# Optimization experiments

Measured on AMD Instinct MI355X. Metric: run time of the kernel, lower is better.

The kernel has to match this reference:

```python
import jax, jax.numpy as jnp
import numpy as np

B, T, V, E, H = 64, 1024, 50000, 256, 512


def setup_inputs() -> dict:
    key = jax.random.key(0)
    ks = jax.random.split(key, 4)
    x = jax.random.randint(ks[0], (B, T), 0, V, dtype=jnp.int32)  # 0 => masked (mask_zero=True)
    initialized_hidden = jnp.zeros((B, H), jnp.float32)
    initialized_cell = jnp.zeros((B, H), jnp.float32)
    emb = jax.random.normal(ks[1], (V, E), jnp.float32) * 0.05
    kernel = jax.random.normal(ks[2], (E, 4 * H), jnp.float32) / np.sqrt(E).astype(np.float32)
    rec_kernel = jax.random.normal(ks[3], (H, 4 * H), jnp.float32) / np.sqrt(H).astype(np.float32)
    # Keras LSTM default: zero bias with unit_forget_bias=True (forget gate bias = 1)
    bias = jnp.concatenate([jnp.zeros(H), jnp.ones(H), jnp.zeros(2 * H)]).astype(jnp.float32)
    return {"x": x, "initialized_hidden": initialized_hidden, "initialized_cell": initialized_cell,
            "emb": emb, "kernel": kernel, "rec_kernel": rec_kernel, "bias": bias}


def _masked_lstm(e, mask, h0, c0, rec_kernel, kernel, bias):
    # Precompute all input projections in one big GEMM: [T, B, 4H]
    xz = jnp.einsum('bte,eg->tbg', e, kernel) + bias
    m_t = mask.T  # [T, B]
    h_units = h0.shape[-1]

    def step(carry, inp):
        h, c = carry
        zx, mt = inp
        z = zx + h @ rec_kernel  # [B, 4H], gate order i,f,c,o (Keras)
        i = jax.nn.sigmoid(z[:, :h_units])
        f = jax.nn.sigmoid(z[:, h_units:2 * h_units])
        g = jnp.tanh(z[:, 2 * h_units:3 * h_units])
        o = jax.nn.sigmoid(z[:, 3 * h_units:])
        c_new = f * c + i * g
        h_new = o * jnp.tanh(c_new)
        m = mt[:, None]
        # masked steps: carry state & output through unchanged (Keras masking semantics)
        h = jnp.where(m, h_new, h)
        c = jnp.where(m, c_new, c)
        return (h, c), h

    (hT, cT), ys = jax.lax.scan(step, (h0, c0), (xz, m_t))
    return ys.transpose(1, 0, 2), hT, cT  # [B,T,H], [B,H], [B,H]


def reference(x, initialized_hidden, initialized_cell, emb, kernel, rec_kernel, bias):
    mask = x != 0  # mask_zero=True
    e = emb[x]     # [B, T, E] embedding lookup
    return _masked_lstm(e, mask, initialized_hidden, initialized_cell, rec_kernel, kernel, bias)
```

## Files before the change

### kernel.cpp

```cpp
#include <hip/hip_runtime.h>
#include <stdint.h>

typedef unsigned short u16;
typedef unsigned int u32;
typedef __attribute__((ext_vector_type(8))) short bf16x8;
typedef __attribute__((ext_vector_type(4))) float f32x4;
typedef __attribute__((ext_vector_type(4))) unsigned int u32x4;
typedef __attribute__((ext_vector_type(2))) unsigned int u32x2;

#define TT 1024
#define BB 64
#define EE 256
#define HH 512
#define GG 2048

#define AS1 __attribute__((address_space(1)))
#define AS3 __attribute__((address_space(3)))

__device__ __forceinline__ float bf2f(u16 h) {
  union { u32 i; float f; } v; v.i = ((u32)h) << 16; return v.f;
}
__device__ __forceinline__ u16 f2bf(float f) {
  union { float f; u32 i; } v; v.f = f;
  u32 b = v.i;
  return (u16)((b + 0x7fffu + ((b >> 16) & 1u)) >> 16);
}
__device__ __forceinline__ float sigm(float x) {
  return 1.f / (1.f + __expf(-x));
}
__device__ __forceinline__ float tanhfast(float x) {
  float e = __expf(2.f * x);
  return 1.f - 2.f / (e + 1.f);
}
__device__ __forceinline__ int cellpos8(int bl, int u) {
  return ((u >> 5) * 32 + ((bl & 7) | (((u >> 3) & 3) << 3))) * 8 + (u & 7);
}
__device__ __forceinline__ int rowbad(u32x4 v, u32 e) {
  return ((((v[0] ^ e) | (v[1] ^ e)) | ((v[2] ^ e) | (v[3] ^ e))) & 0xffffu)
         != 0;
}

#define LOADF(dst, ptr)                                              \
  asm volatile("global_load_dwordx4 %0, %1, off sc0"                 \
               : "=v"(dst) : "v"(ptr))
#define LOADS(dst, ptr)                                              \
  asm volatile("global_load_dwordx4 %0, %1, off sc0 sc1"             \
               : "=v"(dst) : "v"(ptr))
#define WAITV0                                                       \
  asm volatile("s_waitcnt vmcnt(0)" ::: "memory");                   \
  __builtin_amdgcn_sched_barrier(0)

__global__ __launch_bounds__(256) void conv_emb(const float* __restrict__ emb,
                                                u16* __restrict__ embbf) {
  int i = blockIdx.x * 256 + threadIdx.x;
  float4 v = ((const float4*)emb)[i];
  u32x2 p;
  p[0] = (u32)f2bf(v.x) | ((u32)f2bf(v.y) << 16);
  p[1] = (u32)f2bf(v.z) | ((u32)f2bf(v.w) << 16);
  ((u32x2*)embbf)[i] = p;
}

__global__ __launch_bounds__(256) void pack_wk(const float* __restrict__ Wk,
                                               u16* __restrict__ wkp) {
  int idx = blockIdx.x * 256 + threadIdx.x;
  int ct = idx >> 9, ks = (idx >> 6) & 7, l = idx & 63;
  int col = ct * 16 + (l & 15);
  int kb = ks * 32 + ((l >> 4) << 3);
  u32x4 p;
#pragma unroll
  for (int h = 0; h < 4; ++h) {
    u16 a = f2bf(Wk[(size_t)(kb + 2 * h) * GG + col]);
    u16 b = f2bf(Wk[(size_t)(kb + 2 * h + 1) * GG + col]);
    p[h] = (u32)a | ((u32)b << 16);
  }
  *(u32x4*)&wkp[(size_t)idx * 8] = p;
}

__global__ __launch_bounds__(512) void xz_gemm2(
    const int* __restrict__ x, const u16* __restrict__ embbf,
    const u16* __restrict__ wkp, const float* __restrict__ bias,
    u16* __restrict__ xz) {
  extern __shared__ char smg[];
  __shared__ int xidx[16][64];
  __shared__ float biasl[256];
  const int tid = threadIdx.x;
  const int wv = tid >> 6, l = tid & 63;
  const int cb = blockIdx.x & 7;
  const int tg = blockIdx.x >> 3;
  const int mt = wv & 3, nh = wv >> 2;

#pragma unroll
  for (int i = 0; i < 16; ++i)
    __builtin_amdgcn_global_load_lds(
        (AS1 const u32*)(wkp + ((size_t)cb * 65536) +
                         (size_t)(((i * 8 + wv) * 64) + l) * 8),
        (AS3 u32*)(smg + ((i * 8 + wv) << 10)), 16, 0, 0);
  if (tid < 256) {
    int b = tid >> 2, k4 = (tid & 3) << 2;
    int4 v = *(const int4*)&x[(size_t)b * TT + tg * 16 + k4];
    xidx[k4 + 0][b] = v.x; xidx[k4 + 1][b] = v.y;
    xidx[k4 + 2][b] = v.z; xidx[k4 + 3][b] = v.w;
    biasl[tid] = bias[cb * 256 + tid];
  }
  __syncthreads();

  const int row = mt * 16 + (l & 15);
  const int b0 = mt * 16 + ((l >> 4) << 2);
  for (int tl = 0; tl < 16; ++tl) {
    const int xid = xidx[tl][row];
    bf16x8 af[8];
#pragma unroll
    for (int ks = 0; ks < 8; ++ks)
      af[ks] = *(const bf16x8*)&embbf[(size_t)xid * EE + ks * 32 +
                                      ((l >> 4) << 3)];
    const int t = tg * 16 + tl;
#pragma unroll
    for (int nt = 0; nt < 8; ++nt) {
      const int ctl = nh * 8 + nt;
      f32x4 acc = {0.f, 0.f, 0.f, 0.f};
#pragma unroll
      for (int ks = 0; ks < 8; ++ks)
        acc = __builtin_amdgcn_mfma_f32_16x16x32_bf16(
            af[ks], *(const bf16x8*)(smg + (((ctl * 8 + ks) * 64 + l) << 4)),
            acc, 0, 0, 0);
      const int col = cb * 256 + ctl * 16 + (l & 15);
      const float bj = biasl[ctl * 16 + (l & 15)];
      u16 o0 = f2bf(acc[0] + bj), o1 = f2bf(acc[1] + bj);
      u16 o2 = f2bf(acc[2] + bj), o3 = f2bf(acc[3] + bj);
      u32* dst = (u32*)(xz + ((size_t)t * GG + col) * BB + b0);
      dst[0] = (u32)o0 | ((u32)o1 << 16);
      dst[1] = (u32)o2 | ((u32)o3 << 16);
    }
  }
}

__global__ __launch_bounds__(256) void xz_gemm_mfma(
    const int* __restrict__ x, const float* __restrict__ emb,
    const float* __restrict__ Wk, const float* __restrict__ bias,
    u16* __restrict__ xz) {
  extern __shared__ char sm1[];
  bf16x8* Bl = (bf16x8*)sm1;
  __shared__ int xidx[64];
  const int tid = threadIdx.x;
  const int t = blockIdx.x;
  const int w = tid >> 6, l = tid & 63;
  if (tid < 64) xidx[tid] = x[(size_t)tid * TT + t];
  __syncthreads();
  const int row = w * 16 + (l & 15);
  const int xid = xidx[row];
  bf16x8 af[8];
#pragma unroll
  for (int ks = 0; ks < 8; ++ks) {
    int k0 = ks * 32 + ((l >> 4) << 3);
    const float4* p = (const float4*)(emb + (size_t)xid * EE + k0);
    float4 a0 = p[0], a1 = p[1];
    bf16x8 v;
    v[0] = (short)f2bf(a0.x); v[1] = (short)f2bf(a0.y);
    v[2] = (short)f2bf(a0.z); v[3] = (short)f2bf(a0.w);
    v[4] = (short)f2bf(a1.x); v[5] = (short)f2bf(a1.y);
    v[6] = (short)f2bf(a1.z); v[7] = (short)f2bf(a1.w);
    af[ks] = v;
  }
  for (int nb = 0; nb < 8; ++nb) {
    __syncthreads();
    for (int idx = tid; idx < 8192; idx += 256) {
      int nt = idx >> 9, ks = (idx >> 6) & 7, l2 = idx & 63;
      int col = nb * 256 + nt * 16 + (l2 & 15);
      int kb = ks * 32 + ((l2 >> 4) << 3);
      bf16x8 v;
#pragma unroll
      for (int j = 0; j < 8; ++j)
        v[j] = (short)f2bf(Wk[(size_t)(kb + j) * GG + col]);
      Bl[idx] = v;
    }
    __syncthreads();
#pragma unroll 2
    for (int nt = 0; nt < 16; ++nt) {
      f32x4 acc = {0.f, 0.f, 0.f, 0.f};
#pragma unroll
      for (int ks = 0; ks < 8; ++ks)
        acc = __builtin_amdgcn_mfma_f32_16x16x32_bf16(
            af[ks], Bl[(nt * 8 + ks) * 64 + l], acc, 0, 0, 0);
      int col = nb * 256 + nt * 16 + (l & 15);
      float bj = bias[col];
      int b0 = w * 16 + ((l >> 4) << 2);
      u16 o0 = f2bf(acc[0] + bj), o1 = f2bf(acc[1] + bj);
      u16 o2 = f2bf(acc[2] + bj), o3 = f2bf(acc[3] + bj);
      u32* dst = (u32*)(xz + ((size_t)t * GG + col) * BB + b0);
      dst[0] = (u32)o0 | ((u32)o1 << 16);
      dst[1] = (u32)o2 | ((u32)o3 << 16);
    }
  }
}

__global__ __launch_bounds__(512, 2) void lstm_scan12(
    const int* __restrict__ x, const float* __restrict__ h0,
    const float* __restrict__ c0, const float* __restrict__ rec,
    const u16* __restrict__ xz, float* __restrict__ out,
    u32* __restrict__ fastb, u32* __restrict__ slowb) {
  extern __shared__ char sm2[];
  u16* A0 = (u16*)sm2;
  u16* A1 = (u16*)(sm2 + 8192);
  u32* xmask = (u32*)(sm2 + 16384);
  char* ring = sm2 + 17408;
  const int tid = threadIdx.x;
  const int wv = tid >> 6, l = tid & 63;
  const int g = blockIdx.x & 7;
  const int r = blockIdx.x >> 3;
  const int Bg = g * 8;
  const int U0 = r * 64;
  const int q = l & 3;
  const int uoff = (l >> 2) & 3;
  const int u0g = U0 + 8 * wv + uoff;
  const int u1g = u0g + 4;
  const int col0 = q * 512 + u0g;
  const int col1 = q * 512 + u1g;
  const int bl = ((l >> 4) << 2) + q;
  const int blc = bl & 7;
  const bool act = (l < 32);
  const int b = Bg + blc;
  u32* FP0 = fastb + (g * 2 + 0) * 4096;
  u32* FP1 = fastb + (g * 2 + 1) * 4096;
  u32* SP0 = slowb + (g * 2 + 0) * 4096;
  u32* SP1 = slowb + (g * 2 + 1) * 4096;

  const size_t gofs = ((size_t)(wv * 512 + U0 + l)) * BB + Bg;
  if (wv < 4) {
#pragma unroll
    for (int s = 0; s < 7; ++s)
      __builtin_amdgcn_global_load_lds(
          (AS1 const u32*)(xz + (size_t)s * GG * BB + gofs),
          (AS3 u32*)(ring + s * 4096 + wv * 1024), 16, 0, 0);
  }

  bf16x8 bfr0[16], bfr1[16];
#pragma unroll
  for (int ks = 0; ks < 16; ++ks) {
    int kbase = ks * 32 + ((l >> 4) << 3);
#pragma unroll
    for (int j = 0; j < 8; ++j) {
      bfr0[ks][j] = (short)f2bf(rec[(size_t)(kbase + j) * GG + col0]);
      bfr1[ks][j] = (short)f2bf(rec[(size_t)(kbase + j) * GG + col1]);
    }
  }
  if (tid < 256) {
    int bb = tid >> 5, tw = tid & 31;
    u32 mword = 0;
    for (int j = 0; j < 32; ++j)
      mword |= (x[(size_t)(Bg + bb) * TT + tw * 32 + j] != 0 ? 1u : 0u) << j;
    xmask[bb * 32 + tw] = mword;
  }
  float creg0 = c0[(size_t)b * HH + u0g];
  float creg1 = c0[(size_t)b * HH + u1g];
  float hreg0 = h0[(size_t)b * HH + u0g];
  float hreg1 = h0[(size_t)b * HH + u1g];
  asm volatile("s_waitcnt vmcnt(0) lgkmcnt(0)" ::: "memory");
  __syncthreads();

  {
    int uu = tid >> 3, bl2 = tid & 7;
    u32 cell = ((u32)f2bf(h0[(size_t)(Bg + bl2) * HH + U0 + uu]) << 16) | 1u;
    int wp = cellpos8(bl2, U0 + uu);
    __hip_atomic_store(&FP0[wp], cell, __ATOMIC_RELAXED,
                       __HIP_MEMORY_SCOPE_WORKGROUP);
    __hip_atomic_store(&SP0[wp], cell, __ATOMIC_RELAXED,
                       __HIP_MEMORY_SCOPE_AGENT);
  }

  const size_t OFS1 = (size_t)BB * TT * HH;
  const size_t OFS2 = OFS1 + (size_t)BB * HH;
  const int pair = (l & 7) | ((l >> 4) << 3);
  u32 mw = 0;

  for (int t = 0; t < TT; ++t) {
    if ((t & 31) == 0) mw = xmask[blc * 32 + (t >> 5)];
    const bool m = (mw >> (t & 31)) & 1;
    const char* slab = ring + (t & 7) * 4096;
    float xzv[8];
#pragma unroll
    for (int q2 = 0; q2 < 4; ++q2) {
      xzv[q2] = bf2f(*(const u16*)(slab + q2 * 1024 + (8 * wv + uoff) * 16 +
                                   blc * 2));
      xzv[4 + q2] = bf2f(*(const u16*)(slab + q2 * 1024 +
                                       (8 * wv + uoff + 4) * 16 + blc * 2));
    }

    const u32 expect = (u32)(t + 1) & 0xffffu;
    const u32* fb = (t & 1) ? FP1 : FP0;
    const u32* sb = (t & 1) ? SP1 : SP0;
    u32x4 v0, v1;
    LOADF(v0, fb + 8 * tid);
    LOADF(v1, fb + 8 * tid + 4);
    WAITV0;
    int tries = 0;
    while (true) {
      int bad0 = rowbad(v0, expect), bad1 = rowbad(v1, expect);
      if (!__any(bad0 | bad1)) break;
      int a0 = __any(bad0), a1 = __any(bad1);
      __builtin_amdgcn_s_sleep(1);
      ++tries;
      if (a0) LOADF(v0, fb + 8 * tid);
      if (a1) LOADF(v1, fb + 8 * tid + 4);
      if (tries >= 1) {
        u32x4 s0, s1;
        if (a0) LOADS(s0, sb + 8 * tid);
        if (a1) LOADS(s1, sb + 8 * tid + 4);
        WAITV0;
        if (a0 && !rowbad(s0, expect)) v0 = s0;
        if (a1 && !rowbad(s1, expect)) v1 = s1;
      } else {
        WAITV0;
      }
    }
    u16* Ac = (t & 1) ? A1 : A0;
    {
      u32x4 dd;
      dd[0] = (v0[0] >> 16) | (v0[1] & 0xffff0000u);
      dd[1] = (v0[2] >> 16) | (v0[3] & 0xffff0000u);
      dd[2] = (v1[0] >> 16) | (v1[1] & 0xffff0000u);
      dd[3] = (v1[2] >> 16) | (v1[3] & 0xffff0000u);
      *(u32x4*)&Ac[8 * tid] = dd;
    }
    asm volatile("s_waitcnt lgkmcnt(0)" ::: "memory");
    __builtin_amdgcn_s_barrier();
    __builtin_amdgcn_sched_barrier(0);

    if ((t + 7 < TT) && (wv < 4))
      __builtin_amdgcn_global_load_lds(
          (AS1 const u32*)(xz + (size_t)(t + 7) * GG * BB + gofs),
          (AS3 u32*)(ring + ((t + 7) & 7) * 4096 + wv * 1024), 16, 0, 0);

    bf16x8 af[16];
#pragma unroll
    for (int ks = 0; ks < 16; ++ks)
      af[ks] = *(const bf16x8*)&Ac[(ks * 32 + pair) * 8];
    f32x4 acc0 = {0.f, 0.f, 0.f, 0.f}, acc1 = {0.f, 0.f, 0.f, 0.f};
#pragma unroll
    for (int ks = 0; ks < 16; ++ks) {
      acc0 = __builtin_amdgcn_mfma_f32_16x16x32_bf16(af[ks], bfr0[ks], acc0,
                                                     0, 0, 0);
      acc1 = __builtin_amdgcn_mfma_f32_16x16x32_bf16(af[ks], bfr1[ks], acc1,
                                                     0, 0, 0);
    }

    u32* fn = (t & 1) ? FP0 : FP1;
    u32* sn = (t & 1) ? SP0 : SP1;
    const u32 ntag = (u32)(t + 2) & 0xffffu;
    float hosave[2], cosave[2];

#pragma unroll
    for (int ti = 0; ti < 2; ++ti) {
      f32x4 acc = ti ? acc1 : acc0;
      float accLo = (q & 1) ? acc[1] : acc[0];
      float accHi = (q & 1) ? acc[3] : acc[2];
      float sendA = (q & 1) ? acc[0] : acc[1];
      float recvA = __shfl_xor(sendA, 1);
      float sendB = (q & 1) ? acc[2] : acc[3];
      float recvB = __shfl_xor(sendB, 1);
      float k1 = (q & 2) ? accHi : accLo;
      float s2A = (q & 2) ? accLo : accHi;
      float r2A = __shfl_xor(s2A, 2);
      float k2 = (q & 2) ? recvB : recvA;
      float s2B = (q & 2) ? recvA : recvB;
      float r2B = __shfl_xor(s2B, 2);
      float p1 = (q & 1) ? k2 : k1;
      float p2 = (q & 1) ? k1 : k2;
      float p3 = (q & 1) ? r2B : r2A;
      float p4 = (q & 1) ? r2A : r2B;
      float W0 = (q & 2) ? p3 : p1;
      float W1 = (q & 2) ? p4 : p2;
      float W2 = (q & 2) ? p1 : p3;
      float W3 = (q & 2) ? p2 : p4;
      float z0 = W0 + xzv[ti ? 4 : 0];
      float z1 = W1 + xzv[ti ? 5 : 1];
      float z2 = W2 + xzv[ti ? 6 : 2];
      float z3 = W3 + xzv[ti ? 7 : 3];
      float ig = sigm(z0), fg = sigm(z1), gg = tanhfast(z2), og = sigm(z3);
      float cprev = ti ? creg1 : creg0;
      float hprev = ti ? hreg1 : hreg0;
      float cn = fg * cprev + ig * gg;
      float hn = og * tanhfast(cn);
      float ho = m ? hn : hprev;
      float co = m ? cn : cprev;
      if (ti) { creg1 = co; hreg1 = ho; } else { creg0 = co; hreg0 = ho; }
      hosave[ti] = ho; cosave[ti] = co;
      if (act && t < TT - 1) {
        const int u = ti ? u1g : u0g;
        u32 cell = ((u32)f2bf(ho) << 16) | ntag;
        int wp = cellpos8(blc, u);
        __hip_atomic_store(&fn[wp], cell, __ATOMIC_RELAXED,
                           __HIP_MEMORY_SCOPE_WORKGROUP);
        __hip_atomic_store(&sn[wp], cell, __ATOMIC_RELAXED,
                           __HIP_MEMORY_SCOPE_AGENT);
      }
    }
    if (act) {
      __builtin_nontemporal_store(hosave[0],
                                  &out[((size_t)b * TT + t) * HH + u0g]);
      __builtin_nontemporal_store(hosave[1],
                                  &out[((size_t)b * TT + t) * HH + u1g]);
      if (t == TT - 1) {
        out[OFS1 + (size_t)b * HH + u0g] = hosave[0];
        out[OFS1 + (size_t)b * HH + u1g] = hosave[1];
        out[OFS2 + (size_t)b * HH + u0g] = cosave[0];
        out[OFS2 + (size_t)b * HH + u1g] = cosave[1];
      }
    }
  }
}

extern "C" void kernel_launch(void* const* d_in, const int* in_sizes, int n_in,
                              void* d_out, int out_size, void* d_ws,
                              size_t ws_size, hipStream_t stream) {
  const int* x = (const int*)d_in[0];
  const float* h0 = (const float*)d_in[1];
  const float* c0 = (const float*)d_in[2];
  const float* emb = (const float*)d_in[3];
  const float* Wk = (const float*)d_in[4];
  const float* rec = (const float*)d_in[5];
  const float* bias = (const float*)d_in[6];
  float* out = (float*)d_out;
  char* ws = (char*)d_ws;

  const size_t XZ_BYTES = (size_t)TT * GG * BB * 2;
  const size_t EMBBF_BYTES = (size_t)50000 * EE * 2;
  const size_t WKP_BYTES = (size_t)EE * GG * 2;
  u16* xz = (u16*)ws;
  u32* fastb = (u32*)(ws + XZ_BYTES);
  u32* slowb = (u32*)(ws + XZ_BYTES + 262144);
  if (ws_size < XZ_BYTES + 524288) return;

  hipMemsetAsync(fastb, 0, 524288, stream);

  if (ws_size >= XZ_BYTES + 524288 + EMBBF_BYTES + WKP_BYTES) {
    u16* embbf = (u16*)(ws + XZ_BYTES + 524288);
    u16* wkp = (u16*)(ws + XZ_BYTES + 524288 + EMBBF_BYTES);
    conv_emb<<<12500, 256, 0, stream>>>(emb, embbf);
    pack_wk<<<256, 256, 0, stream>>>(Wk, wkp);
    hipFuncSetAttribute((const void*)xz_gemm2,
                        hipFuncAttributeMaxDynamicSharedMemorySize, 131072);
    xz_gemm2<<<512, 512, 131072, stream>>>(x, embbf, wkp, bias, xz);
  } else {
    hipFuncSetAttribute((const void*)xz_gemm_mfma,
                        hipFuncAttributeMaxDynamicSharedMemorySize, 131072);
    xz_gemm_mfma<<<TT, 256, 131072, stream>>>(x, emb, Wk, bias, xz);
  }

  hipFuncSetAttribute((const void*)lstm_scan12,
                      hipFuncAttributeMaxDynamicSharedMemorySize, 50176);
  lstm_scan12<<<64, 512, 50176, stream>>>(x, h0, c0, rec, xz, out, fastb,
                                          slowb);
}
```

Baseline: 2.899 ms.

## Detect XCD co-location at runtime and route h exchange accordingly

Result: slower. 5.957 ms (+105.5%).

```diff
diff --git a/kernel.cpp b/kernel.cpp
--- a/kernel.cpp
+++ b/kernel.cpp
@@ -193,20 +193,22 @@
   }
 }
 
-__global__ __launch_bounds__(512, 2) void lstm_scan12(
+__global__ __launch_bounds__(512, 2) void lstm_scan13(
     const int* __restrict__ x, const float* __restrict__ h0,
     const float* __restrict__ c0, const float* __restrict__ rec,
     const u16* __restrict__ xz, float* __restrict__ out,
-    u32* __restrict__ fastb, u32* __restrict__ slowb) {
+    u32* __restrict__ fastb, u32* __restrict__ slowb,
+    u32* __restrict__ xcdtab) {
   extern __shared__ char sm2[];
   u16* A0 = (u16*)sm2;
   u16* A1 = (u16*)(sm2 + 8192);
   u32* xmask = (u32*)(sm2 + 16384);
   char* ring = sm2 + 17408;
+  __shared__ u32 myxcdL;
   const int tid = threadIdx.x;
   const int wv = tid >> 6, l = tid & 63;
-  const int g = blockIdx.x & 7;
-  const int r = blockIdx.x >> 3;
+  const int g = blockIdx.x >> 3;
+  const int r = blockIdx.x & 7;
   const int Bg = g * 8;
   const int U0 = r * 64;
   const int q = l & 3;
@@ -224,6 +226,15 @@
   u32* SP0 = slowb + (g * 2 + 0) * 4096;
   u32* SP1 = slowb + (g * 2 + 1) * 4096;
 
+  if (tid == 0) {
+    u32 xcd;
+    asm volatile("s_getreg_b32 %0, hwreg(HW_REG_XCC_ID)" : "=s"(xcd));
+    xcd = (xcd & 7u) | 0x100u;
+    myxcdL = xcd;
+    __hip_atomic_store(&xcdtab[blockIdx.x], xcd, __ATOMIC_RELAXED,
+                       __HIP_MEMORY_SCOPE_AGENT);
+  }
+
   const size_t gofs = ((size_t)(wv * 512 + U0 + l)) * BB + Bg;
   if (wv < 4) {
 #pragma unroll
@@ -270,6 +281,9 @@
   const size_t OFS1 = (size_t)BB * TT * HH;
   const size_t OFS2 = OFS1 + (size_t)BB * HH;
   const int pair = (l & 7) | ((l >> 4) << 3);
+  const u32 myx = myxcdL;
+  const int prodbid = (g << 3) | wv;
+  bool fastok = false;
   u32 mw = 0;
 
   for (int t = 0; t < TT; ++t) {
@@ -289,29 +303,52 @@
     const u32* fb = (t & 1) ? FP1 : FP0;
     const u32* sb = (t & 1) ? SP1 : SP0;
     u32x4 v0, v1;
-    LOADF(v0, fb + 8 * tid);
-    LOADF(v1, fb + 8 * tid + 4);
-    WAITV0;
-    int tries = 0;
-    while (true) {
-      int bad0 = rowbad(v0, expect), bad1 = rowbad(v1, expect);
-      if (!__any(bad0 | bad1)) break;
-      int a0 = __any(bad0), a1 = __any(bad1);
-      __builtin_amdgcn_s_sleep(1);
-      ++tries;
-      if (a0) LOADF(v0, fb + 8 * tid);
-      if (a1) LOADF(v1, fb + 8 * tid + 4);
-      if (tries >= 1) {
-        u32x4 s0, s1;
-        if (a0) LOADS(s0, sb + 8 * tid);
-        if (a1) LOADS(s1, sb + 8 * tid + 4);
-        WAITV0;
-        if (a0 && !rowbad(s0, expect)) v0 = s0;
-        if (a1 && !rowbad(s1, expect)) v1 = s1;
-      } else {
+    if (fastok) {
+      LOADF(v0, fb + 8 * tid);
+      LOADF(v1, fb + 8 * tid + 4);
+      WAITV0;
+      int tries = 0;
+      while (true) {
+        int bad0 = rowbad(v0, expect), bad1 = rowbad(v1, expect);
+        if (!__any(bad0 | bad1)) break;
+        int a0 = __any(bad0), a1 = __any(bad1);
+        __builtin_amdgcn_s_sleep(1);
+        ++tries;
+        if (a0) LOADF(v0, fb + 8 * tid);
+        if (a1) LOADF(v1, fb + 8 * tid + 4);
+        if (tries >= 64) {
+          u32x4 s0, s1;
+          if (a0) LOADS(s0, sb + 8 * tid);
+          if (a1) LOADS(s1, sb + 8 * tid + 4);
+          WAITV0;
+          if (a0 && !rowbad(s0, expect)) v0 = s0;
+          if (a1 && !rowbad(s1, expect)) v1 = s1;
+        } else {
+          WAITV0;
+        }
+      }
+    } else {
+      LOADS(v0, sb + 8 * tid);
+      LOADS(v1, sb + 8 * tid + 4);
+      WAITV0;
+      while (true) {
+        int bad0 = rowbad(v0, expect), bad1 = rowbad(v1, expect);
+        if (!__any(bad0 | bad1)) break;
+        int a0 = __any(bad0), a1 = __any(bad1);
+        __builtin_amdgcn_s_sleep(1);
+        if (a0) LOADS(v0, sb + 8 * tid);
+        if (a1) LOADS(v1, sb + 8 * tid + 4);
         WAITV0;
       }
-    }
+      if (t == 0) {
+        u32 ptag;
+        asm volatile("global_load_dword %0, %1, off sc0 sc1"
+                     : "=v"(ptag) : "v"(xcdtab + prodbid));
+        asm volatile("s_waitcnt vmcnt(0)" ::: "memory");
+        fastok = (ptag == myx);
+      }
+    }
+
     u16* Ac = (t & 1) ? A1 : A0;
     {
       u32x4 dd;
@@ -394,17 +431,24 @@
                            __HIP_MEMORY_SCOPE_AGENT);
       }
     }
-    if (act) {
-      __builtin_nontemporal_store(hosave[0],
-                                  &out[((size_t)b * TT + t) * HH + u0g]);
-      __builtin_nontemporal_store(hosave[1],
-                                  &out[((size_t)b * TT + t) * HH + u1g]);
-      if (t == TT - 1) {
-        out[OFS1 + (size_t)b * HH + u0g] = hosave[0];
-        out[OFS1 + (size_t)b * HH + u1g] = hosave[1];
-        out[OFS2 + (size_t)b * HH + u0g] = cosave[0];
-        out[OFS2 + (size_t)b * HH + u1g] = cosave[1];
-      }
+    if (t == TT - 1 && act) {
+      out[((size_t)b * TT + (TT - 1)) * HH + u0g] = hosave[0];
+      out[((size_t)b * TT + (TT - 1)) * HH + u1g] = hosave[1];
+      out[OFS1 + (size_t)b * HH + u0g] = hosave[0];
+      out[OFS1 + (size_t)b * HH + u1g] = hosave[1];
+      out[OFS2 + (size_t)b * HH + u0g] = cosave[0];
+      out[OFS2 + (size_t)b * HH + u1g] = cosave[1];
+    }
+    if (t > 0 && (((t - 1) & 7) == r)) {
+      int b2 = tid >> 6, k = tid & 63;
+      int cb2 = ((k >> 2) << 8) + ((b2 + ((k & 3) << 3)) << 3);
+      const bf16x8 hv = *(const bf16x8*)&Ac[cb2];
+      float o8[8];
+#pragma unroll
+      for (int j = 0; j < 8; ++j) o8[j] = bf2f((u16)hv[j]);
+      float* dst = out + ((size_t)(Bg + b2) * TT + (t - 1)) * HH + k * 8;
+      *(f32x4*)dst = *(const f32x4*)&o8[0];
+      *(f32x4*)(dst + 4) = *(const f32x4*)&o8[4];
     }
   }
 }
@@ -423,18 +467,20 @@
   char* ws = (char*)d_ws;
 
   const size_t XZ_BYTES = (size_t)TT * GG * BB * 2;
+  const size_t EXCH_BYTES = 524288 + 4096;
   const size_t EMBBF_BYTES = (size_t)50000 * EE * 2;
   const size_t WKP_BYTES = (size_t)EE * GG * 2;
   u16* xz = (u16*)ws;
   u32* fastb = (u32*)(ws + XZ_BYTES);
   u32* slowb = (u32*)(ws + XZ_BYTES + 262144);
-  if (ws_size < XZ_BYTES + 524288) return;
-
-  hipMemsetAsync(fastb, 0, 524288, stream);
-
-  if (ws_size >= XZ_BYTES + 524288 + EMBBF_BYTES + WKP_BYTES) {
-    u16* embbf = (u16*)(ws + XZ_BYTES + 524288);
-    u16* wkp = (u16*)(ws + XZ_BYTES + 524288 + EMBBF_BYTES);
+  u32* xcdtab = (u32*)(ws + XZ_BYTES + 524288);
+  if (ws_size < XZ_BYTES + EXCH_BYTES) return;
+
+  hipMemsetAsync(fastb, 0, EXCH_BYTES, stream);
+
+  if (ws_size >= XZ_BYTES + EXCH_BYTES + EMBBF_BYTES + WKP_BYTES) {
+    u16* embbf = (u16*)(ws + XZ_BYTES + EXCH_BYTES);
+    u16* wkp = (u16*)(ws + XZ_BYTES + EXCH_BYTES + EMBBF_BYTES);
     conv_emb<<<12500, 256, 0, stream>>>(emb, embbf);
     pack_wk<<<256, 256, 0, stream>>>(Wk, wkp);
     hipFuncSetAttribute((const void*)xz_gemm2,
@@ -446,8 +492,8 @@
     xz_gemm_mfma<<<TT, 256, 131072, stream>>>(x, emb, Wk, bias, xz);
   }
 
-  hipFuncSetAttribute((const void*)lstm_scan12,
+  hipFuncSetAttribute((const void*)lstm_scan13,
                       hipFuncAttributeMaxDynamicSharedMemorySize, 50176);
-  lstm_scan12<<<64, 512, 50176, stream>>>(x, h0, c0, rec, xz, out, fastb,
-                                          slowb);
-}
+  lstm_scan13<<<64, 512, 50176, stream>>>(x, h0, c0, rec, xz, out, fastb,
+                                          slowb, xcdtab);
+}
```
